# Optimization experiments

Measured on AMD Instinct MI355X. Metric: run time of the kernel, lower is better.

## Reference

```python
import jax, jax.numpy as jnp
import numpy as np

S, FEAT, D, H, L, DFF, C = 1024, 64, 512, 8, 2, 2048, 10
DB = D // 4  # distance-bias MLP hidden
NFREQ = D // 6  # 85 -> 6*85=510 dims, padded to 512
EPS = 1e-5


def _layernorm(x, g, b):
    mu = jnp.mean(x, axis=-1, keepdims=True)
    var = jnp.mean(jnp.square(x - mu), axis=-1, keepdims=True)
    return (x - mu) * jax.lax.rsqrt(var + EPS) * g + b


def setup_inputs() -> dict:
    key = jax.random.key(0)
    ks = iter(jax.random.split(key, 40))
    def w(shape, scale=0.02):
        return (jax.random.normal(next(ks), shape, jnp.float32) * scale)
    inp = {
        'features': jax.random.normal(next(ks), (S, FEAT), jnp.float32),
        'positions': jax.random.uniform(next(ks), (S, 3), jnp.float32),
        'freq_bands': jnp.asarray(10.0 ** np.linspace(0.0, 10.0, NFREQ), jnp.float32),
        'in_w': w((FEAT, D)), 'in_b': jnp.zeros((D,), jnp.float32),
        'qw': w((L, D, D)), 'qb': jnp.zeros((L, D), jnp.float32),
        'kw': w((L, D, D)), 'kb': jnp.zeros((L, D), jnp.float32),
        'vw': w((L, D, D)), 'vb': jnp.zeros((L, D), jnp.float32),
        'ow': w((L, D, D)), 'ob': jnp.zeros((L, D), jnp.float32),
        'db1w': w((L, 1, DB), 0.5), 'db1b': jnp.zeros((L, DB), jnp.float32),
        'db2w': w((L, DB, H), 0.1), 'db2b': jnp.zeros((L, H), jnp.float32),
        'n1g': jnp.ones((L, D), jnp.float32), 'n1b': jnp.zeros((L, D), jnp.float32),
        'n2g': jnp.ones((L, D), jnp.float32), 'n2b': jnp.zeros((L, D), jnp.float32),
        'f1w': w((L, D, DFF)), 'f1b': jnp.zeros((L, DFF), jnp.float32),
        'f2w': w((L, DFF, D)), 'f2b': jnp.zeros((L, D), jnp.float32),
        'c1w': w((D, D // 2)), 'c1b': jnp.zeros((D // 2,), jnp.float32),
        'c2w': w((D // 2, C)), 'c2b': jnp.zeros((C,), jnp.float32),
    }
    return inp


def _forward(features, positions, freq_bands, in_w, in_b, qw, qb, kw, kb, vw, vb,
             ow, ob, db1w, db1b, db2w, db2b, n1g, n1b, n2g, n2b,
             f1w, f1b, f2w, f2b, c1w, c1b, c2w, c2b):
    d_model = in_w.shape[1]
    nhead = db2w.shape[-1]
    head_dim = d_model // nhead
    scale = 1.0 / np.sqrt(head_dim)

    x = features[None] @ in_w + in_b            # [1, S, D]
    pos = positions[None]                        # [1, S, 3]

    # 3D sinusoidal positional encoding: [sin0,cos0,sin1,cos1,sin2,cos2]
    enc = []
    for i in range(3):
        cs = pos[..., i:i + 1] * freq_bands      # [1, S, NFREQ] (broadcast)
        enc.append(jnp.sin(cs))
        enc.append(jnp.cos(cs))
    pe = jnp.concatenate(enc, axis=-1)           # [1, S, 6*NFREQ]
    if pe.shape[-1] > d_model:
        pe = pe[..., :d_model]
    elif pe.shape[-1] < d_model:
        pe = jnp.pad(pe, ((0, 0), (0, 0), (0, d_model - pe.shape[-1])))
    x = x + pe

    # pairwise distances [1, S, S, 1]; safe sqrt (zero grad on diagonal)
    diff = pos[:, :, None, :] - pos[:, None, :, :]
    sq = jnp.sum(jnp.square(diff), axis=-1, keepdims=True)
    dist = jnp.sqrt(jnp.where(sq > 0, sq, 1.0)) * (sq > 0)

    n_layers = qw.shape[0]
    seq = x.shape[1]
    for l in range(n_layers):
        q = (x @ qw[l] + qb[l]).reshape(1, seq, nhead, head_dim)
        k = (x @ kw[l] + kb[l]).reshape(1, seq, nhead, head_dim)
        v = (x @ vw[l] + vb[l]).reshape(1, seq, nhead, head_dim)
        scores = jnp.einsum('bihd,bjhd->bhij', q, k) * scale  # [1,H,S,S]
        hbias = jax.nn.relu(dist @ db1w[l] + db1b[l])          # [1,S,S,DB]
        bias = jnp.einsum('bijc,ch->bhij', hbias, db2w[l]) + db2b[l][None, :, None, None]
        attn = jax.nn.softmax(scores + bias, axis=-1)
        out = jnp.einsum('bhij,bjhd->bihd', attn, v).reshape(1, seq, d_model)
        out = out @ ow[l] + ob[l]
        x = _layernorm(x + out, n1g[l], n1b[l])
        ffn = jax.nn.relu(x @ f1w[l] + f1b[l]) @ f2w[l] + f2b[l]
        x = _layernorm(x + ffn, n2g[l], n2b[l])

    pooled = jnp.mean(x, axis=1)                 # [1, D]
    return jax.nn.relu(pooled @ c1w + c1b) @ c2w + c2b  # [1, C]


def reference(features, positions, freq_bands, in_w, in_b, qw, qb, kw, kb, vw, vb,
              ow, ob, db1w, db1b, db2w, db2b, n1g, n1b, n2g, n2b,
              f1w, f1b, f2w, f2b, c1w, c1b, c2w, c2b):
    return _forward(features, positions, freq_bands, in_w, in_b, qw, qb, kw, kb, vw, vb,
                    ow, ob, db1w, db1b, db2w, db2b, n1g, n1b, n2g, n2b,
                    f1w, f1b, f2w, f2b, c1w, c1b, c2w, c2b)
```

## Files before the change

kernel.cpp:

```cpp
#include <hip/hip_runtime.h>

namespace {
constexpr int kS   = 1024;
constexpr int kD   = 512;
constexpr int kDFF = 2048;
constexpr int kNF  = 85;
}

typedef __attribute__((ext_vector_type(8))) short bhalf8_t;
typedef _Float16 half8_t __attribute__((ext_vector_type(8)));
typedef __attribute__((ext_vector_type(4))) float f32x4_t;

__device__ __forceinline__ float wave_sum(float v) {
#pragma unroll
    for (int o = 1; o < 64; o <<= 1) v += __shfl_xor(v, o, 64);
    return v;
}
__device__ __forceinline__ unsigned short f2h(float f) {
    _Float16 h = (_Float16)f;
    return __builtin_bit_cast(unsigned short, h);
}
__device__ __forceinline__ float h2f(unsigned short u) {
    return (float)__builtin_bit_cast(_Float16, u);
}

__device__ __forceinline__ void tr_tile32(const float* __restrict__ in,
                                          unsigned short* __restrict__ out,
                                          int N, int K, int k0, int n0, int t,
                                          float* tile )
{
    int r = t >> 3, c4 = (t & 7) * 4;
    float4 v = *reinterpret_cast<const float4*>(&in[(long)(k0 + r) * N + n0 + c4]);
    tile[r * 33 + c4] = v.x; tile[r * 33 + c4 + 1] = v.y;
    tile[r * 33 + c4 + 2] = v.z; tile[r * 33 + c4 + 3] = v.w;
    __syncthreads();
    int nr = t >> 3, kq = (t & 7) * 4;
    unsigned short h[4];
#pragma unroll
    for (int j = 0; j < 4; ++j) h[j] = f2h(tile[(kq + j) * 33 + nr]);
    *reinterpret_cast<ushort4*>(&out[(long)(n0 + nr) * K + k0 + kq]) =
        make_ushort4(h[0], h[1], h[2], h[3]);
}

__global__ __launch_bounds__(256)
void prep_k(const float* __restrict__ feat, const float* __restrict__ pos,
            const float* __restrict__ fb, const float* __restrict__ in_w,
            const float* __restrict__ in_b, float* __restrict__ x,
            unsigned short* __restrict__ xb, float* __restrict__ dist,
            const float* __restrict__ qw, const float* __restrict__ kw,
            const float* __restrict__ vw, const float* __restrict__ ow,
            unsigned short* __restrict__ qwb, unsigned short* __restrict__ kwb,
            unsigned short* __restrict__ vwb, unsigned short* __restrict__ owb,
            const float* __restrict__ f1w, unsigned short* __restrict__ f1wb,
            const float* __restrict__ f2w, unsigned short* __restrict__ f2wb,
            const float* __restrict__ a_, const float* __restrict__ b_,
            const float* __restrict__ w2, const float* __restrict__ b2,
            float* __restrict__ bp_out, float* __restrict__ Atab,
            float* __restrict__ Btab)
{
    __shared__ float smem[1056];
    int bid = blockIdx.x;
    int t = threadIdx.x;
    if (bid < 256) {
        int s0 = bid * 4;
        smem[t] = feat[s0 * 64 + t];
        __syncthreads();
        float b0 = in_b[t], b1 = in_b[t + 256];
        float a0[4] = {b0, b0, b0, b0}, a1[4] = {b1, b1, b1, b1};
#pragma unroll 4
        for (int c = 0; c < 64; ++c) {
            float w0 = in_w[c * kD + t], w1 = in_w[c * kD + 256 + t];
#pragma unroll
            for (int r = 0; r < 4; ++r) {
                a0[r] = fmaf(smem[r * 64 + c], w0, a0[r]);
                a1[r] = fmaf(smem[r * 64 + c], w1, a1[r]);
            }
        }
#pragma unroll
        for (int r = 0; r < 4; ++r) {
            int s = s0 + r;
            float pe0 = 0.f, pe1 = 0.f;
            int d = t;
            if (d < 6 * kNF) {
                int seg = d / kNF, idx = d - seg * kNF;
                float cs = pos[s * 3 + (seg >> 1)] * fb[idx];
                pe0 = (seg & 1) ? cosf(cs) : sinf(cs);
            }
            d = t + 256;
            if (d < 6 * kNF) {
                int seg = d / kNF, idx = d - seg * kNF;
                float cs = pos[s * 3 + (seg >> 1)] * fb[idx];
                pe1 = (seg & 1) ? cosf(cs) : sinf(cs);
            }
            float o0 = a0[r] + pe0, o1 = a1[r] + pe1;
            x[s * kD + t]        = o0;
            x[s * kD + 256 + t]  = o1;
            xb[s * kD + t]       = f2h(o0);
            xb[s * kD + 256 + t] = f2h(o1);
        }
    } else if (bid < 1280) {
        int i = bid - 256;
        float px = pos[i * 3], py = pos[i * 3 + 1], pz = pos[i * 3 + 2];
        for (int j = t; j < kS; j += 256) {
            float dx = px - pos[j * 3], dy = py - pos[j * 3 + 1], dz = pz - pos[j * 3 + 2];
            float sq = dx * dx + dy * dy + dz * dz;
            dist[(long)i * kS + j] = sq > 0.f ? sqrtf(sq) : 0.f;
        }
    } else if (bid < 7424) {
        int idx = bid - 1280;
        if (idx < 2048) {
            int zz = idx >> 8, rem = idx & 255;
            int mat = zz >> 1, layer = zz & 1;
            const float* in = (mat == 0) ? qw : (mat == 1) ? kw : (mat == 2) ? vw : ow;
            unsigned short* out = (mat == 0) ? qwb : (mat == 1) ? kwb : (mat == 2) ? vwb : owb;
            tr_tile32(in + (long)layer * 262144, out + (long)layer * 262144,
                      512, 512, (rem & 15) * 32, (rem >> 4) * 32, t, smem);
        } else if (idx < 4096) {
            int l = idx - 2048;
            int z = l >> 10;
            tr_tile32(f1w + (long)z * 1048576, f1wb + (long)z * 1048576,
                      2048, 512, (l & 15) * 32, ((l >> 4) & 63) * 32, t, smem);
        } else {
            int l = idx - 4096;
            int z = l >> 10;
            tr_tile32(f2w + (long)z * 1048576, f2wb + (long)z * 1048576,
                      512, 2048, (l & 63) * 32, ((l >> 6) & 15) * 32, t, smem);
        }
    } else {
        int l = bid - 7424;
        int seg = l % 129, ly = l / 129;
        const float* ap = a_ + ly * 128;
        const float* bpp = b_ + ly * 128;
        const float* w2p = w2 + ly * 1024;
        const float* b2p = b2 + ly * 8;
        float* At = Atab + ly * 1040;
        float* Bt = Btab + ly * 1040;

        if (t < 128) {
            float a = ap[t], b = bpp[t];
            smem[t] = (a != 0.f) ? (-b / a) : 3.0e38f;
        }
        __syncthreads();
        for (int ksz = 2; ksz <= 128; ksz <<= 1) {
            for (int j = ksz >> 1; j > 0; j >>= 1) {
                if (t < 128) {
                    int ixj = t ^ j;
                    if (ixj > t) {
                        bool up = ((t & ksz) == 0);
                        float x0 = smem[t], x1 = smem[ixj];
                        if ((x0 > x1) == up) { smem[t] = x1; smem[ixj] = x0; }
                    }
                }
                __syncthreads();
            }
        }
        float m;
        if (seg == 0)        m = smem[0] - 1.0f;
        else if (seg == 128) m = smem[127] + 1.0f;
        else                 m = 0.5f * (smem[seg - 1] + smem[seg]);
        if (seg == 0 && t < 128) bp_out[ly * 128 + t] = smem[t];
        __syncthreads();

        int h = t & 7, cg = t >> 3;
        float A = 0.f, B = 0.f;
#pragma unroll
        for (int j = 0; j < 4; ++j) {
            int c = cg * 4 + j;
            float a = ap[c], b = bpp[c];
            if (fmaf(a, m, b) > 0.f) {
                float w = w2p[c * 8 + h];
                A = fmaf(a, w, A);
                B = fmaf(b, w, B);
            }
        }
#pragma unroll
        for (int off = 8; off < 64; off <<= 1) {
            A += __shfl_xor(A, off, 64);
            B += __shfl_xor(B, off, 64);
        }
        int w = t >> 6, lane = t & 63;
        if (lane < 8) { smem[w * 8 + lane] = A; smem[32 + w * 8 + lane] = B; }
        __syncthreads();
        if (t < 8) {
            float At_ = smem[t] + smem[8 + t] + smem[16 + t] + smem[24 + t];
            float Bt_ = smem[32 + t] + smem[40 + t] + smem[48 + t] + smem[56 + t];
            At[seg * 8 + t] = At_;
            Bt[seg * 8 + t] = Bt_ + b2p[t];
        }
    }
}

constexpr int ASZ2 = 64 * 64;
constexpr int BSZ2 = 128 * 64;

constexpr int BKp = 72;
constexpr int ASZ = 64 * BKp;
constexpr int BSZ = 128 * BKp;

__device__ __forceinline__ void gload16(const unsigned short* g, unsigned short* l) {
    __builtin_amdgcn_global_load_lds(
        (const __attribute__((address_space(1))) unsigned int*)g,
        (__attribute__((address_space(3))) unsigned int*)l, 16, 0, 0);
}

template<int K>
__device__ __forceinline__ void gemm_core(
    const unsigned short* __restrict__ Ap, const unsigned short* __restrict__ Bp,
    int lda, int ldb, int bm, int bn, int tid,
    unsigned short* __restrict__ As, unsigned short* __restrict__ Bs,
    f32x4_t acc[2][4])
{
    int w = tid >> 6, lane = tid & 63, quad = lane >> 4, l16 = lane & 15;
    int wm = (w >> 1) * 32, wn = (w & 1) * 64;
    int lr = lane >> 3;
    int sw = (lane & 7) ^ lr;

    const unsigned short* pa  = Ap + (long)(bm + w * 16 + lr) * lda + sw * 8;
    const unsigned short* pa2 = pa + (long)8 * lda;
    const unsigned short* pb  = Bp + (long)(bn + w * 32 + lr) * ldb + sw * 8;

    auto stage = [&](int t) {
        int buf = t % 3;
        unsigned short* as = As + buf * ASZ2 + w * 16 * 64;
        unsigned short* bs = Bs + buf * BSZ2 + w * 32 * 64;
        int k0 = t * 64;
        gload16(pa + k0, as);
        gload16(pa2 + k0, as + 8 * 64);
#pragma unroll
        for (int j = 0; j < 4; ++j)
            gload16(pb + (long)(j * 8) * ldb + k0, bs + j * 8 * 64);
    };

    constexpr int NT = K / 64;
    stage(0);
    if (NT > 1) stage(1);
    int r7 = l16 & 7;
#pragma unroll
    for (int t = 0; t < NT; ++t) {
        if (t + 1 < NT) asm volatile("s_waitcnt vmcnt(6)" ::: "memory");
        else            asm volatile("s_waitcnt vmcnt(0)" ::: "memory");
        __builtin_amdgcn_s_barrier();
        __builtin_amdgcn_sched_barrier(0);
        if (t + 2 < NT) stage(t + 2);
        const unsigned short* as = As + (t % 3) * ASZ2;
        const unsigned short* bs = Bs + (t % 3) * BSZ2;
#pragma unroll
        for (int kq = 0; kq < 2; ++kq) {
            int slot = ((kq * 4 + quad) ^ r7) * 8;
            bhalf8_t af[2], bf[4];
#pragma unroll
            for (int i = 0; i < 2; ++i)
                af[i] = *reinterpret_cast<const bhalf8_t*>(
                    &as[(wm + i * 16 + l16) * 64 + slot]);
#pragma unroll
            for (int j = 0; j < 4; ++j)
                bf[j] = *reinterpret_cast<const bhalf8_t*>(
                    &bs[(wn + j * 16 + l16) * 64 + slot]);
#pragma unroll
            for (int i = 0; i < 2; ++i)
#pragma unroll
                for (int j = 0; j < 4; ++j)
                    acc[i][j] = __builtin_amdgcn_mfma_f32_16x16x32_f16(
                        __builtin_bit_cast(half8_t, af[i]), __builtin_bit_cast(half8_t, bf[j]),
                        acc[i][j], 0, 0, 0);
        }
    }
}

__global__ __launch_bounds__(256, 2)
void qkv_bias_k(const unsigned short* __restrict__ xb,
                const unsigned short* __restrict__ qwb, const unsigned short* __restrict__ kwb,
                const unsigned short* __restrict__ vwb,
                const float* __restrict__ qbias, const float* __restrict__ kbias,
                const float* __restrict__ vbias,
                unsigned short* __restrict__ qb2, unsigned short* __restrict__ kb2,
                unsigned short* __restrict__ vtb,
                const float* __restrict__ dist, const float* __restrict__ bp,
                const float* __restrict__ Atab, const float* __restrict__ Btab,
                unsigned short* __restrict__ bmap, unsigned int* __restrict__ cnt)
{
    __shared__ __align__(16) unsigned short smem[3 * ASZ2 + 3 * BSZ2];
    int bid = blockIdx.x;
    int tid = threadIdx.x;
    if (bid < 192) {
        int z = bid >> 6, rem = bid & 63;
        int bm = (rem & 15) * 64, bn = (rem >> 4) * 128;
        const unsigned short* Bp = (z == 1) ? kwb : (z == 2) ? vwb : qwb;
        const float* bias = (z == 1) ? kbias : (z == 2) ? vbias : qbias;
        f32x4_t acc[2][4] = {};
        gemm_core<512>(xb, Bp, 512, 512, bm, bn, tid, smem, smem + 3 * ASZ2, acc);

        int w = tid >> 6, lane = tid & 63, quad = lane >> 4, l16 = lane & 15;
        int wm = (w >> 1) * 32, wn = (w & 1) * 64;
        if (z == 2) {
            __syncthreads();
            unsigned short* T = smem;
#pragma unroll
            for (int j = 0; j < 4; ++j) {
                int ln = wn + j * 16 + l16;
                float bv = bias[bn + ln];
#pragma unroll
                for (int i = 0; i < 2; ++i)
#pragma unroll
                    for (int r = 0; r < 4; ++r)
                        T[ln * BKp + wm + i * 16 + quad * 4 + r] =
                            f2h((acc[i][j][r] + bv) * 1024.f);
            }
            __syncthreads();
            int nr = tid >> 1, mc = (tid & 1) * 32;
            int gn = bn + nr;
            unsigned short* dst = vtb + (long)(gn >> 6) * 65536
                                + (long)(gn & 63) * 1024 + bm + mc;
#pragma unroll
            for (int jj = 0; jj < 4; ++jj)
                *reinterpret_cast<bhalf8_t*>(dst + jj * 8) =
                    *reinterpret_cast<const bhalf8_t*>(&T[nr * BKp + mc + jj * 8]);
        } else {
#pragma unroll
            for (int j = 0; j < 4; ++j) {
                int n = bn + wn + j * 16 + l16;
                float bv = bias[n];
                unsigned short* dst = ((z == 1) ? kb2 : qb2)
                    + (long)(n >> 6) * 131072 + (n & 63);
#pragma unroll
                for (int i = 0; i < 2; ++i)
#pragma unroll
                    for (int r = 0; r < 4; ++r) {
                        int m = bm + wm + i * 16 + quad * 4 + r;
                        float s = acc[i][j][r] + bv;
                        unsigned short hi = f2h(s);
                        dst[(long)m * 128]      = hi;
                        dst[(long)m * 128 + 64] = (z == 0) ? f2h(s - h2f(hi)) : hi;
                    }
            }
        }
    } else {
        if (bid == 192 && tid < 8) cnt[tid] = 0;
        float* fs = reinterpret_cast<float*>(smem);
        float* bps = fs;
        float* Ah  = fs + 128;
        float* Bh  = fs + 1160;
        unsigned short* perm = smem + 4384;
        int t = tid;
        if (t < 128) bps[t] = bp[t];
        for (int i = t; i < 1032; i += 256) { Ah[i] = Atab[i]; Bh[i] = Btab[i]; }
        __syncthreads();

        long gm = bid - 192;
        int gn0 = t * 4;
        float4 d4 = *reinterpret_cast<const float4*>(dist + gm * 1024 + gn0);
        float dv[4] = {d4.x, d4.y, d4.z, d4.w};
        int seg[4];
#pragma unroll
        for (int j = 0; j < 4; ++j) {
            float tv = dv[j];
            int lo = 0, hi = 128;
            while (lo < hi) { int mid = (lo + hi) >> 1; if (bps[mid] < tv) lo = mid + 1; else hi = mid; }
            seg[j] = lo;
        }
        int zz = gn0 >> 7, nb = (gn0 >> 4) & 7, c4 = gn0 & 15;
        int pb0 = zz * 136 + nb;
#pragma unroll
        for (int h = 0; h < 8; ++h) {
            unsigned short* ph = perm + h * 1088 + pb0;
#pragma unroll
            for (int j = 0; j < 4; ++j)
                ph[(c4 + j) * 8] =
                    f2h(fmaf(Ah[seg[j] * 8 + h], dv[j], Bh[seg[j] * 8 + h]));
        }
        __syncthreads();
#pragma unroll
        for (int it = 0; it < 4; ++it) {
            int idx = it * 2048 + t * 8;
            int h   = idx >> 10;
            int off = idx & 1023;
            int z2  = off >> 7, r = off & 127;
            *reinterpret_cast<bhalf8_t*>(bmap + (long)h * 1048576 + gm * 1024 + off) =
                *reinterpret_cast<const bhalf8_t*>(&perm[h * 1088 + z2 * 136 + r]);
        }
    }
}

__global__ __launch_bounds__(256, 2)
void bgemm_ffn1_k(const unsigned short* __restrict__ A,
                  const unsigned short* __restrict__ B,
                  const float* __restrict__ bias,
                  unsigned short* __restrict__ hb)
{
    __shared__ __align__(16) unsigned short smem[3 * ASZ2 + 3 * BSZ2];
    int tid = threadIdx.x;
    int bm = blockIdx.x * 64, bn = blockIdx.y * 128;
    f32x4_t acc[2][4] = {};
    gemm_core<512>(A, B, 512, 512, bm, bn, tid, smem, smem + 3 * ASZ2, acc);

    int w = tid >> 6, lane = tid & 63, quad = lane >> 4, l16 = lane & 15;
    int wm = (w >> 1) * 32, wn = (w & 1) * 64;
#pragma unroll
    for (int j = 0; j < 4; ++j) {
        int n = bn + wn + j * 16 + l16;
        float bv = bias[n];
#pragma unroll
        for (int i = 0; i < 2; ++i)
#pragma unroll
            for (int r = 0; r < 4; ++r) {
                int m = bm + wm + i * 16 + quad * 4 + r;
                hb[(long)m * kDFF + n] = f2h(fmaxf(acc[i][j][r] + bv, 0.f));
            }
    }
}

template<int K>
__global__ __launch_bounds__(256, 2)
void bgemm_k(const unsigned short* __restrict__ A, const unsigned short* __restrict__ B,
             int N, int lda, int ldb, unsigned short* __restrict__ Cpart)
{
    __shared__ __align__(16) unsigned short smem[3 * ASZ2 + 3 * BSZ2];
    int tid = threadIdx.x;
    int ks = blockIdx.z;
    const unsigned short* Ap = A + (long)ks * K;
    const unsigned short* Bp = B + (long)ks * K;
    int bm = blockIdx.x * 64, bn = blockIdx.y * 128;
    f32x4_t acc[2][4] = {};
    gemm_core<K>(Ap, Bp, lda, ldb, bm, bn, tid, smem, smem + 3 * ASZ2, acc);

    int w = tid >> 6, lane = tid & 63, quad = lane >> 4, l16 = lane & 15;
    int wm = (w >> 1) * 32, wn = (w & 1) * 64;
    unsigned short* Cp = Cpart + (long)ks * kS * N;
#pragma unroll
    for (int i = 0; i < 2; ++i)
#pragma unroll
        for (int j = 0; j < 4; ++j)
#pragma unroll
            for (int r = 0; r < 4; ++r) {
                int m = bm + wm + i * 16 + quad * 4 + r;
                int n = bn + wn + j * 16 + l16;
                Cp[(long)m * N + n] = f2h(acc[i][j][r]);
            }
}

__global__ __launch_bounds__(256, 2)
void bgemm_oproj_k(const unsigned short* __restrict__ po,
                   const float* __restrict__ pm, const float* __restrict__ pl,
                   const unsigned short* __restrict__ Bw,
                   unsigned short* __restrict__ Cpart)
{
    __shared__ __align__(16) unsigned short As[2 * ASZ];
    __shared__ __align__(16) unsigned short Bs[2 * BSZ];
    __shared__ float wz_s[2][64][9];
    __shared__ float inv_s[2][64];

    int tid = threadIdx.x;
    int ks = blockIdx.z;
    int bm = blockIdx.x * 64, bn = blockIdx.y * 128;
    int h0 = ks * 2;

    int br = tid >> 1, bc = (tid & 1) * 32;
    {
        const unsigned short* pb = Bw + (long)(bn + br) * 512 + ks * 128 + bc;
#pragma unroll
        for (int t = 0; t < 2; ++t) {
            bhalf8_t v0 = *reinterpret_cast<const bhalf8_t*>(pb + t * 64);
            bhalf8_t v1 = *reinterpret_cast<const bhalf8_t*>(pb + t * 64 + 8);
            bhalf8_t v2 = *reinterpret_cast<const bhalf8_t*>(pb + t * 64 + 16);
            bhalf8_t v3 = *reinterpret_cast<const bhalf8_t*>(pb + t * 64 + 24);
            unsigned short* bs = Bs + t * BSZ;
            *reinterpret_cast<bhalf8_t*>(&bs[br * BKp + bc])      = v0;
            *reinterpret_cast<bhalf8_t*>(&bs[br * BKp + bc + 8])  = v1;
            *reinterpret_cast<bhalf8_t*>(&bs[br * BKp + bc + 16]) = v2;
            *reinterpret_cast<bhalf8_t*>(&bs[br * BKp + bc + 24]) = v3;
        }
    }

    if (tid < 128) {
        int t = tid >> 6, r = tid & 63;
        long sidx = (long)(h0 + t) * 1024 + bm + r;
        float m[8], M = -3.0e38f;
#pragma unroll
        for (int z = 0; z < 8; ++z) { m[z] = pm[z * 8192 + sidx]; M = fmaxf(M, m[z]); }
        float lt = 0.f;
#pragma unroll
        for (int z = 0; z < 8; ++z) {
            float w = __expf(m[z] - M);
            wz_s[t][r][z] = w;
            lt = fmaf(pl[z * 8192 + sidx], w, lt);
        }
        inv_s[t][r] = 1.f / lt;
    }
    __syncthreads();

    int ar = tid >> 2, ac = (tid & 3) * 16;
#pragma unroll
    for (int t = 0; t < 2; ++t) {
        float inv = inv_s[t][ar];
        const unsigned short* p = po + ((long)(h0 + t) * 1024 + bm + ar) * 64 + ac;
        float acc[16] = {};
#pragma unroll
        for (int z = 0; z < 8; ++z) {
            float w = wz_s[t][ar][z];
            bhalf8_t v0 = *reinterpret_cast<const bhalf8_t*>(p + (long)z * 524288);
            bhalf8_t v1 = *reinterpret_cast<const bhalf8_t*>(p + (long)z * 524288 + 8);
#pragma unroll
            for (int j = 0; j < 8; ++j) {
                acc[j]     = fmaf(h2f((unsigned short)v0[j]), w, acc[j]);
                acc[8 + j] = fmaf(h2f((unsigned short)v1[j]), w, acc[8 + j]);
            }
        }
        unsigned short* as = As + t * ASZ;
#pragma unroll
        for (int j = 0; j < 16; ++j)
            as[ar * BKp + ac + j] = f2h(acc[j] * inv);
    }
    __syncthreads();

    int w = tid >> 6, lane = tid & 63, quad = lane >> 4, l16 = lane & 15;
    int wm = (w >> 1) * 32, wn = (w & 1) * 64;
    f32x4_t accf[2][4] = {};
#pragma unroll
    for (int t = 0; t < 2; ++t) {
        const unsigned short* as = As + t * ASZ;
        const unsigned short* bs = Bs + t * BSZ;
#pragma unroll
        for (int kq = 0; kq < 2; ++kq) {
            bhalf8_t af[2], bf[4];
#pragma unroll
            for (int i = 0; i < 2; ++i)
                af[i] = *reinterpret_cast<const bhalf8_t*>(
                    &as[(wm + i * 16 + l16) * BKp + kq * 32 + quad * 8]);
#pragma unroll
            for (int j = 0; j < 4; ++j)
                bf[j] = *reinterpret_cast<const bhalf8_t*>(
                    &bs[(wn + j * 16 + l16) * BKp + kq * 32 + quad * 8]);
#pragma unroll
            for (int i = 0; i < 2; ++i)
#pragma unroll
                for (int j = 0; j < 4; ++j)
                    accf[i][j] = __builtin_amdgcn_mfma_f32_16x16x32_f16(
                        __builtin_bit_cast(half8_t, af[i]), __builtin_bit_cast(half8_t, bf[j]),
                        accf[i][j], 0, 0, 0);
        }
    }

    unsigned short* Cp = Cpart + (long)ks * kS * 512;
#pragma unroll
    for (int i = 0; i < 2; ++i)
#pragma unroll
        for (int j = 0; j < 4; ++j)
#pragma unroll
            for (int r = 0; r < 4; ++r) {
                int m = bm + wm + i * 16 + quad * 4 + r;
                int n = bn + wn + j * 16 + l16;
                Cp[(long)m * 512 + n] = f2h(accf[i][j][r]);
            }
}

__global__ __launch_bounds__(256, 3)
void flash_part_k(const unsigned short* __restrict__ qb2, const unsigned short* __restrict__ kb2,
                  const unsigned short* __restrict__ vtb, const unsigned short* __restrict__ bmap,
                  unsigned short* __restrict__ po, float* __restrict__ pm, float* __restrict__ pl)
{
    constexpr int KP = 136;
    __shared__ __align__(16) unsigned short Klds[128 * KP];
    __shared__ __align__(16) unsigned short Vlds[64 * KP];

    int tid = threadIdx.x;
    int w    = tid >> 6;
    int lane = tid & 63;
    int quad = lane >> 4, l16 = lane & 15;

    int wg  = blockIdx.x;
    int lin = (wg & 7) * 128 + (wg >> 3);
    int qbg = lin & 15;
    int h   = (lin >> 4) & 7;
    int z   = lin >> 7;
    int qb  = qbg * 4 + w;
    int bm  = qb * 16;
    int k0  = z * 128;

    const unsigned short* Qh = qb2 + (long)h * 131072;
    const unsigned short* Kh = kb2 + (long)h * 131072;
    const unsigned short* Vh = vtb + (long)h * 65536;
    const unsigned short* Bm = bmap + (long)h * 1048576;

    {
        int kr = tid >> 1, kc = (tid & 1) * 64;
#pragma unroll
        for (int j = 0; j < 8; ++j)
            *reinterpret_cast<bhalf8_t*>(&Klds[kr * KP + kc + j * 8]) =
                *reinterpret_cast<const bhalf8_t*>(&Kh[(long)(k0 + kr) * 128 + kc + j * 8]);
        int vr = tid >> 2, vc = (tid & 3) * 32;
#pragma unroll
        for (int j = 0; j < 4; ++j)
            *reinterpret_cast<bhalf8_t*>(&Vlds[vr * KP + vc + j * 8]) =
                *reinterpret_cast<const bhalf8_t*>(&Vh[(long)vr * 1024 + k0 + vc + j * 8]);
    }

    bhalf8_t aq[4];
#pragma unroll
    for (int kq = 0; kq < 4; ++kq)
        aq[kq] = *reinterpret_cast<const bhalf8_t*>(
            &Qh[(long)(bm + l16) * 128 + kq * 32 + quad * 8]);
    bhalf8_t bias8[4];
#pragma unroll
    for (int r = 0; r < 4; ++r) {
        int gm = bm + quad * 4 + r;
        bias8[r] = *reinterpret_cast<const bhalf8_t*>(
            &Bm[(long)gm * 1024 + z * 128 + l16 * 8]);
    }

    __syncthreads();

    f32x4_t sacc[8] = {};
#pragma unroll
    for (int kq = 0; kq < 4; ++kq) {
        bhalf8_t bk[8];
#pragma unroll
        for (int nb = 0; nb < 8; ++nb)
            bk[nb] = *reinterpret_cast<const bhalf8_t*>(
                &Klds[(nb * 16 + l16) * KP + kq * 32 + quad * 8]);
#pragma unroll
        for (int nb = 0; nb < 8; ++nb)
            sacc[nb] = __builtin_amdgcn_mfma_f32_16x16x32_f16(
                __builtin_bit_cast(half8_t, aq[kq]), __builtin_bit_cast(half8_t, bk[nb]),
                sacc[nb], 0, 0, 0);
    }

    float m_r[4] = {-3.0e38f, -3.0e38f, -3.0e38f, -3.0e38f};
#pragma unroll
    for (int nb = 0; nb < 8; ++nb)
#pragma unroll
        for (int r = 0; r < 4; ++r) {
            float bias = h2f((unsigned short)bias8[r][nb]);
            float s = fmaf(sacc[nb][r], 0.125f, bias);
            sacc[nb][r] = s;
            m_r[r] = fmaxf(m_r[r], s);
        }
#pragma unroll
    for (int r = 0; r < 4; ++r) {
        float m_ = m_r[r];
#pragma unroll
        for (int off = 1; off < 16; off <<= 1) m_ = fmaxf(m_, __shfl_xor(m_, off, 64));
        m_r[r] = m_;
    }

    __syncthreads();

    unsigned short* Ps = Klds + w * 16 * KP;
    float l_r[4];
#pragma unroll
    for (int r = 0; r < 4; ++r) {
        int row = quad * 4 + r;
        float mN = m_r[r];
        float s_ = 0.f;
#pragma unroll
        for (int nb = 0; nb < 8; ++nb) {
            float p = __expf(sacc[nb][r] - mN);
            Ps[row * KP + nb * 16 + l16] = f2h(p * 16384.f);
            s_ += p;
        }
#pragma unroll
        for (int off = 1; off < 16; off <<= 1) s_ += __shfl_xor(s_, off, 64);
        l_r[r] = s_;
    }

    long sbase = (((long)z * 8 + h) * 64 + qb) * 16;
    if (l16 == 0) {
#pragma unroll
        for (int r = 0; r < 4; ++r) {
            pm[sbase + quad * 4 + r] = m_r[r];
            pl[sbase + quad * 4 + r] = l_r[r];
        }
    }

    f32x4_t oacc[4] = {};
#pragma unroll
    for (int kq2 = 0; kq2 < 4; ++kq2) {
        bhalf8_t ap = *reinterpret_cast<const bhalf8_t*>(&Ps[l16 * KP + kq2 * 32 + quad * 8]);
#pragma unroll
        for (int j2 = 0; j2 < 4; ++j2) {
            bhalf8_t bv = *reinterpret_cast<const bhalf8_t*>(
                &Vlds[(j2 * 16 + l16) * KP + kq2 * 32 + quad * 8]);
            oacc[j2] = __builtin_amdgcn_mfma_f32_16x16x32_f16(
                __builtin_bit_cast(half8_t, ap), __builtin_bit_cast(half8_t, bv),
                oacc[j2], 0, 0, 0);
        }
    }

    unsigned short* pob = po + sbase * 64;
#pragma unroll
    for (int j2 = 0; j2 < 4; ++j2)
#pragma unroll
        for (int r = 0; r < 4; ++r)
            pob[(quad * 4 + r) * 64 + j2 * 16 + l16] =
                f2h(oacc[j2][r] * (1.f / 16777216.f));
}

__global__ __launch_bounds__(256)
void add_ln_fused_k(const unsigned short* __restrict__ part, float* __restrict__ x,
                    const float* __restrict__ bias,
                    const float* __restrict__ g, const float* __restrict__ b,
                    unsigned short* __restrict__ xb, int splitk)
{
    __shared__ float sm[4];
    int row = blockIdx.x, t = threadIdx.x;
    const long MN = (long)kS * kD;
    float* xr = x + (long)row * kD;
    float s0 = 0.f, s1 = 0.f;
    const unsigned short* pr = part + (long)row * kD;
    for (int sl = 0; sl < splitk; ++sl) {
        s0 += h2f(pr[(long)sl * MN + t]);
        s1 += h2f(pr[(long)sl * MN + t + 256]);
    }
    s0 += bias[t] + xr[t];
    s1 += bias[t + 256] + xr[t + 256];
    float sum = wave_sum(s0 + s1);
    if ((t & 63) == 0) sm[t >> 6] = sum;
    __syncthreads();
    sum = sm[0] + sm[1] + sm[2] + sm[3];
    float mu = sum * (1.f / kD);
    float d0 = s0 - mu, d1 = s1 - mu;
    __syncthreads();
    float vs = wave_sum(d0 * d0 + d1 * d1);
    if ((t & 63) == 0) sm[t >> 6] = vs;
    __syncthreads();
    vs = sm[0] + sm[1] + sm[2] + sm[3];
    float rs = rsqrtf(vs * (1.f / kD) + 1e-5f);
    float o0 = fmaf(d0 * rs, g[t], b[t]);
    float o1 = fmaf(d1 * rs, g[t + 256], b[t + 256]);
    xr[t]       = o0;
    xr[t + 256] = o1;
    unsigned short* xrow = xb + (long)row * 512;
    xrow[t]       = f2h(o0);
    xrow[t + 256] = f2h(o1);
}

__global__ __launch_bounds__(256)
void pool_head_k(const float* __restrict__ x, float* __restrict__ partial,
                 float* __restrict__ h1g, unsigned int* __restrict__ cnt2,
                 const float* __restrict__ c1w, const float* __restrict__ c1b,
                 const float* __restrict__ c2w, const float* __restrict__ c2b,
                 float* __restrict__ out)
{
    __shared__ float pooled[kD];
    __shared__ int flag;
    int t = threadIdx.x;
    int bid = blockIdx.x;
    int cb = bid & 1, rb = bid >> 1;
    int col = cb * 256 + t;
    float s = 0.f;
    for (int r = rb * 128; r < rb * 128 + 128; ++r) s += x[(long)r * kD + col];
    partial[rb * kD + col] = s;

    __threadfence();
    if (t == 0) {
        atomicAdd(&cnt2[0], 1u);
        while (atomicAdd(&cnt2[0], 0u) < 16u) {}
    }
    __syncthreads();
    __threadfence();

    {
        float p0 = 0.f, p1 = 0.f;
#pragma unroll
        for (int r = 0; r < 8; ++r) {
            p0 += partial[r * kD + t];
            p1 += partial[r * kD + t + 256];
        }
        pooled[t]       = p0 * (1.0f / kS);
        pooled[t + 256] = p1 * (1.0f / kS);
    }
    __syncthreads();

    {
        int c = bid * 16 + (t >> 4);
        int sub = t & 15;
        float a = 0.f;
        for (int f = sub; f < kD; f += 16)
            a = fmaf(pooled[f], c1w[(long)f * 256 + c], a);
#pragma unroll
        for (int o = 1; o < 16; o <<= 1) a += __shfl_xor(a, o, 64);
        if (sub == 0) h1g[c] = fmaxf(a + c1b[c], 0.f);
    }

    __threadfence();
    if (t == 0) flag = (atomicAdd(&cnt2[1], 1u) == 15u);
    __syncthreads();
    if (!flag) return;
    __threadfence();

    if (t < 160) {
        int c = t >> 4, sub = t & 15;
        float a = 0.f;
        for (int f = sub; f < 256; f += 16)
            a = fmaf(h1g[f], c2w[(long)f * 10 + c], a);
#pragma unroll
        for (int o = 1; o < 16; o <<= 1) a += __shfl_xor(a, o, 64);
        if (sub == 0) out[c] = a + c2b[c];
    }
}

extern "C" void kernel_launch(void* const* d_in, const int* in_sizes, int n_in,
                              void* d_out, int out_size, void* d_ws, size_t ws_size,
                              hipStream_t stream)
{
    (void)in_sizes; (void)n_in; (void)out_size; (void)ws_size;
    const float* features = (const float*)d_in[0];
    const float* positions= (const float*)d_in[1];
    const float* fb       = (const float*)d_in[2];
    const float* in_w     = (const float*)d_in[3];
    const float* in_b     = (const float*)d_in[4];
    const float* qw  = (const float*)d_in[5];
    const float* qb  = (const float*)d_in[6];
    const float* kw  = (const float*)d_in[7];
    const float* kb  = (const float*)d_in[8];
    const float* vw  = (const float*)d_in[9];
    const float* vb  = (const float*)d_in[10];
    const float* ow  = (const float*)d_in[11];
    const float* ob  = (const float*)d_in[12];
    const float* db1w= (const float*)d_in[13];
    const float* db1b= (const float*)d_in[14];
    const float* db2w= (const float*)d_in[15];
    const float* db2b= (const float*)d_in[16];
    const float* n1g = (const float*)d_in[17];
    const float* n1b = (const float*)d_in[18];
    const float* n2g = (const float*)d_in[19];
    const float* n2b = (const float*)d_in[20];
    const float* f1w = (const float*)d_in[21];
    const float* f1b = (const float*)d_in[22];
    const float* f2w = (const float*)d_in[23];
    const float* f2b = (const float*)d_in[24];
    const float* c1w = (const float*)d_in[25];
    const float* c1b = (const float*)d_in[26];
    const float* c2w = (const float*)d_in[27];
    const float* c2b = (const float*)d_in[28];

    float* ws = (float*)d_ws;
    const long SD = (long)kS * kD;
    float* x      = ws;
    float* dist   = ws + 3 * SD;
    float* part_f = ws + 5 * SD;
    float* bpw    = ws + 17 * SD;
    float* Atab   = bpw + 256;
    float* Btab   = Atab + 2080;
    float* partial= Btab + 2080;

    unsigned short* part16 = (unsigned short*)part_f;
    unsigned short* po     = (unsigned short*)part_f;
    float* pmv = part_f + 2162688;
    float* plv = pmv + 65536;
    unsigned int* cnt2 = (unsigned int*)(plv + 65536);
    float* h1g = (float*)(cnt2 + 16);
    unsigned short* part16b = (unsigned short*)(part_f + 2294048);

    unsigned short* ub = (unsigned short*)(ws + 17 * SD + 8512);
    unsigned short* xb   = ub;
    unsigned short* qb2  = ub   + 1048576;
    unsigned short* kb2  = qb2  + 1048576;
    unsigned short* vtb  = kb2  + 1048576;
    unsigned short* hb   = vtb  + 524288;
    unsigned short* qwb  = hb   + 2097152;
    unsigned short* kwb  = qwb  + 524288;
    unsigned short* vwb  = kwb  + 524288;
    unsigned short* owb  = vwb  + 524288;
    unsigned short* f1wb = owb  + 524288;
    unsigned short* f2wb = f1wb + 2097152;
    unsigned short* bmap = f2wb + 2097152;

    prep_k<<<7682, 256, 0, stream>>>(features, positions, fb, in_w, in_b, x, xb,
                                     dist, qw, kw, vw, ow, qwb, kwb, vwb, owb,
                                     f1w, f1wb, f2w, f2wb,
                                     db1w, db1b, db2w, db2b, bpw, Atab, Btab);

    for (int l = 0; l < 2; ++l) {
        qkv_bias_k<<<1216, 256, 0, stream>>>(
            xb, qwb + l * 262144, kwb + l * 262144, vwb + l * 262144,
            qb + l * kD, kb + l * kD, vb + l * kD, qb2, kb2, vtb,
            dist, bpw + l * 128, Atab + l * 1040, Btab + l * 1040, bmap, cnt2);

        flash_part_k<<<1024, 256, 0, stream>>>(
            qb2, kb2, vtb, bmap, po, pmv, plv);

        bgemm_oproj_k<<<dim3(16, 4, 4), 256, 0, stream>>>(
            po, pmv, plv, owb + l * 262144, part16b);
        add_ln_fused_k<<<kS, 256, 0, stream>>>(
            part16b, x, ob + l * kD, n1g + l * kD, n1b + l * kD, xb, 4);

        bgemm_ffn1_k<<<dim3(16, 16), 256, 0, stream>>>(
            xb, f1wb + l * 1048576, f1b + l * kDFF, hb);

        bgemm_k<512><<<dim3(16, 4, 4), 256, 0, stream>>>(
            hb, f2wb + l * 1048576, 512, 2048, 2048, part16);
        add_ln_fused_k<<<kS, 256, 0, stream>>>(
            part16, x, f2b + l * kD, n2g + l * kD, n2b + l * kD, xb, 4);
    }

    pool_head_k<<<16, 256, 0, stream>>>(x, partial, h1g, cnt2,
                                        c1w, c1b, c2w, c2b, (float*)d_out);
}
```

Baseline: 268.8 us.

## Compute pairwise distances on the fly in bias kernel; widen flash blocks to 512 threads

Removes the precomputed S×S distance matrix from prep_k and instead recomputes pairwise distances from positions staged in shared memory inside qkv_bias_k, which avoids writing and reading a 4 MB buffer. The input projection in prep_k now handles 8 rows per block instead of 4, halving its block count. flash_part_k moves to 512-thread blocks with 8 waves sharing each K/V tile, which halves the grid and changes the cooperative load pattern. Risks: the distance is recomputed for each layer (twice), the larger flash blocks may cut occupancy, and the posl shared-memory offset must not overlap other shared data.

```diff
diff --git a/kernel.cpp b/kernel.cpp
--- a/kernel.cpp
+++ b/kernel.cpp
@@ -46,7 +46,7 @@
 void prep_k(const float* __restrict__ feat, const float* __restrict__ pos,
             const float* __restrict__ fb, const float* __restrict__ in_w,
             const float* __restrict__ in_b, float* __restrict__ x,
-            unsigned short* __restrict__ xb, float* __restrict__ dist,
+            unsigned short* __restrict__ xb,
             const float* __restrict__ qw, const float* __restrict__ kw,
             const float* __restrict__ vw, const float* __restrict__ ow,
             unsigned short* __restrict__ qwb, unsigned short* __restrict__ kwb,
@@ -61,23 +61,26 @@
     __shared__ float smem[1056];
     int bid = blockIdx.x;
     int t = threadIdx.x;
-    if (bid < 256) {
-        int s0 = bid * 4;
-        smem[t] = feat[s0 * 64 + t];
+    if (bid < 128) {
+        int s0 = bid * 8;
+        smem[t]       = feat[s0 * 64 + t];
+        smem[256 + t] = feat[s0 * 64 + 256 + t];
         __syncthreads();
         float b0 = in_b[t], b1 = in_b[t + 256];
-        float a0[4] = {b0, b0, b0, b0}, a1[4] = {b1, b1, b1, b1};
+        float a0[8], a1[8];
+#pragma unroll
+        for (int r = 0; r < 8; ++r) { a0[r] = b0; a1[r] = b1; }
 #pragma unroll 4
         for (int c = 0; c < 64; ++c) {
             float w0 = in_w[c * kD + t], w1 = in_w[c * kD + 256 + t];
 #pragma unroll
-            for (int r = 0; r < 4; ++r) {
+            for (int r = 0; r < 8; ++r) {
                 a0[r] = fmaf(smem[r * 64 + c], w0, a0[r]);
                 a1[r] = fmaf(smem[r * 64 + c], w1, a1[r]);
             }
         }
 #pragma unroll
-        for (int r = 0; r < 4; ++r) {
+        for (int r = 0; r < 8; ++r) {
             int s = s0 + r;
             float pe0 = 0.f, pe1 = 0.f;
             int d = t;
@@ -98,16 +101,8 @@
             xb[s * kD + t]       = f2h(o0);
             xb[s * kD + 256 + t] = f2h(o1);
         }
-    } else if (bid < 1280) {
-        int i = bid - 256;
-        float px = pos[i * 3], py = pos[i * 3 + 1], pz = pos[i * 3 + 2];
-        for (int j = t; j < kS; j += 256) {
-            float dx = px - pos[j * 3], dy = py - pos[j * 3 + 1], dz = pz - pos[j * 3 + 2];
-            float sq = dx * dx + dy * dy + dz * dz;
-            dist[(long)i * kS + j] = sq > 0.f ? sqrtf(sq) : 0.f;
-        }
-    } else if (bid < 7424) {
-        int idx = bid - 1280;
+    } else if (bid < 6272) {
+        int idx = bid - 128;
         if (idx < 2048) {
             int zz = idx >> 8, rem = idx & 255;
             int mat = zz >> 1, layer = zz & 1;
@@ -127,7 +122,7 @@
                       512, 2048, (l & 63) * 32, ((l >> 6) & 15) * 32, t, smem);
         }
     } else {
-        int l = bid - 7424;
+        int l = bid - 6272;
         int seg = l % 129, ly = l / 129;
         const float* ap = a_ + ly * 128;
         const float* bpp = b_ + ly * 128;
@@ -275,7 +270,7 @@
                 const float* __restrict__ vbias,
                 unsigned short* __restrict__ qb2, unsigned short* __restrict__ kb2,
                 unsigned short* __restrict__ vtb,
-                const float* __restrict__ dist, const float* __restrict__ bp,
+                const float* __restrict__ pos, const float* __restrict__ bp,
                 const float* __restrict__ Atab, const float* __restrict__ Btab,
                 unsigned short* __restrict__ bmap, unsigned int* __restrict__ cnt)
 {
@@ -341,19 +336,27 @@
         float* Ah  = fs + 128;
         float* Bh  = fs + 1160;
         unsigned short* perm = smem + 4384;
+        float* posl = reinterpret_cast<float*>(smem + 13088);
         int t = tid;
         if (t < 128) bps[t] = bp[t];
         for (int i = t; i < 1032; i += 256) { Ah[i] = Atab[i]; Bh[i] = Btab[i]; }
+        for (int i = t; i < 3072; i += 256) posl[i] = pos[i];
         __syncthreads();
 
         long gm = bid - 192;
+        float px = posl[gm * 3], py = posl[gm * 3 + 1], pz = posl[gm * 3 + 2];
         int gn0 = t * 4;
-        float4 d4 = *reinterpret_cast<const float4*>(dist + gm * 1024 + gn0);
-        float dv[4] = {d4.x, d4.y, d4.z, d4.w};
+        float dv[4];
         int seg[4];
 #pragma unroll
         for (int j = 0; j < 4; ++j) {
-            float tv = dv[j];
+            int jj = gn0 + j;
+            float dx = px - posl[jj * 3];
+            float dy = py - posl[jj * 3 + 1];
+            float dz = pz - posl[jj * 3 + 2];
+            float sq = dx * dx + dy * dy + dz * dz;
+            float tv = sq > 0.f ? sqrtf(sq) : 0.f;
+            dv[j] = tv;
             int lo = 0, hi = 128;
             while (lo < hi) { int mid = (lo + hi) >> 1; if (bps[mid] < tv) lo = mid + 1; else hi = mid; }
             seg[j] = lo;
@@ -553,7 +556,7 @@
             }
 }
 
-__global__ __launch_bounds__(256, 3)
+__global__ __launch_bounds__(512, 4)
 void flash_part_k(const unsigned short* __restrict__ qb2, const unsigned short* __restrict__ kb2,
                   const unsigned short* __restrict__ vtb, const unsigned short* __restrict__ bmap,
                   unsigned short* __restrict__ po, float* __restrict__ pm, float* __restrict__ pl)
@@ -568,11 +571,11 @@
     int quad = lane >> 4, l16 = lane & 15;
 
     int wg  = blockIdx.x;
-    int lin = (wg & 7) * 128 + (wg >> 3);
-    int qbg = lin & 15;
-    int h   = (lin >> 4) & 7;
-    int z   = lin >> 7;
-    int qb  = qbg * 4 + w;
+    int lin = (wg & 7) * 64 + (wg >> 3);
+    int qbg = lin & 7;
+    int h   = (lin >> 3) & 7;
+    int z   = lin >> 6;
+    int qb  = qbg * 8 + w;
     int bm  = qb * 16;
     int k0  = z * 128;
 
@@ -582,14 +585,14 @@
     const unsigned short* Bm = bmap + (long)h * 1048576;
 
     {
-        int kr = tid >> 1, kc = (tid & 1) * 64;
-#pragma unroll
-        for (int j = 0; j < 8; ++j)
+        int kr = tid >> 2, kc = (tid & 3) * 32;
+#pragma unroll
+        for (int j = 0; j < 4; ++j)
             *reinterpret_cast<bhalf8_t*>(&Klds[kr * KP + kc + j * 8]) =
                 *reinterpret_cast<const bhalf8_t*>(&Kh[(long)(k0 + kr) * 128 + kc + j * 8]);
-        int vr = tid >> 2, vc = (tid & 3) * 32;
-#pragma unroll
-        for (int j = 0; j < 4; ++j)
+        int vr = tid >> 3, vc = (tid & 7) * 16;
+#pragma unroll
+        for (int j = 0; j < 2; ++j)
             *reinterpret_cast<bhalf8_t*>(&Vlds[vr * KP + vc + j * 8]) =
                 *reinterpret_cast<const bhalf8_t*>(&Vh[(long)vr * 1024 + k0 + vc + j * 8]);
     }
@@ -836,7 +839,6 @@
     float* ws = (float*)d_ws;
     const long SD = (long)kS * kD;
     float* x      = ws;
-    float* dist   = ws + 3 * SD;
     float* part_f = ws + 5 * SD;
     float* bpw    = ws + 17 * SD;
     float* Atab   = bpw + 256;
@@ -865,8 +867,8 @@
     unsigned short* f2wb = f1wb + 2097152;
     unsigned short* bmap = f2wb + 2097152;
 
-    prep_k<<<7682, 256, 0, stream>>>(features, positions, fb, in_w, in_b, x, xb,
-                                     dist, qw, kw, vw, ow, qwb, kwb, vwb, owb,
+    prep_k<<<6530, 256, 0, stream>>>(features, positions, fb, in_w, in_b, x, xb,
+                                     qw, kw, vw, ow, qwb, kwb, vwb, owb,
                                      f1w, f1wb, f2w, f2wb,
                                      db1w, db1b, db2w, db2b, bpw, Atab, Btab);
 
@@ -874,9 +876,9 @@
         qkv_bias_k<<<1216, 256, 0, stream>>>(
             xb, qwb + l * 262144, kwb + l * 262144, vwb + l * 262144,
             qb + l * kD, kb + l * kD, vb + l * kD, qb2, kb2, vtb,
-            dist, bpw + l * 128, Atab + l * 1040, Btab + l * 1040, bmap, cnt2);
-
-        flash_part_k<<<1024, 256, 0, stream>>>(
+            positions, bpw + l * 128, Atab + l * 1040, Btab + l * 1040, bmap, cnt2);
+
+        flash_part_k<<<512, 512, 0, stream>>>(
             qb2, kb2, vtb, bmap, po, pmv, plv);
 
         bgemm_oproj_k<<<dim3(16, 4, 4), 256, 0, stream>>>(
```

Measured after the change: 279.9 us. 1.04x slower.
